# Performance work log

Hardware: AMD Instinct MI355X
Metric: run time of the kernel (lower is better)

## Reference

```python
import jax, jax.numpy as jnp
import numpy as np
import math

H = 12  # heads (init kwarg)
KEEP_RATE = 0.7  # forward arg keep_rate (< 1 -> token pruning path)


def setup_inputs() -> dict:
    key = jax.random.key(0)
    k0, k1, k2 = jax.random.split(key, 3)
    b, n, c = 32, 577, 768  # ViT-B/16 @ 384px: 576 patches + CLS
    x = jax.random.normal(k0, (b, n, c), dtype=jnp.float32)
    # nn.Linear(dim, dim*3) and nn.Linear(dim, dim); kaiming-ish scale
    W_qkv = jax.random.normal(k1, (c, 3 * c), dtype=jnp.float32) / np.sqrt(c).astype(np.float32)
    b_qkv = jnp.zeros((3 * c,), dtype=jnp.float32)
    W_out = jax.random.normal(k2, (c, c), dtype=jnp.float32) / np.sqrt(c).astype(np.float32)
    b_out = jnp.zeros((c,), dtype=jnp.float32)
    return {"x": x, "keep_rate": KEEP_RATE, "W_qkv": W_qkv, "b_qkv": b_qkv,
            "W_out": W_out, "b_out": b_out}


def reference(x, keep_rate, W_qkv, b_qkv, W_out, b_out):
    b, n, c = x.shape
    d = c // H
    scale = (c / H) ** -0.5
    # qkv projection + split into heads: 'b n (h d) -> b h n d'
    qkv = x @ W_qkv + b_qkv                      # [b, n, 3c]
    q, k, v = jnp.split(qkv, 3, axis=-1)
    split_heads = lambda t: t.reshape(b, n, H, d).transpose(0, 2, 1, 3)
    q, k, v = split_heads(q), split_heads(k), split_heads(v)
    dots = jnp.einsum('bhid,bhjd->bhij', q, k) * scale   # [b,h,n,n]
    attention = jax.nn.softmax(dots, axis=-1)
    out = jnp.einsum('bhij,bhjd->bhid', attention, v)    # [b,h,n,d]
    out = out.transpose(0, 2, 1, 3).reshape(b, n, c)     # 'b h n d -> b n (h d)'
    out = out @ W_out + b_out                            # to_out (dropout=0)
    final_tokens = n - 1
    if keep_rate < 1:
        final_tokens = math.ceil(keep_rate * final_tokens)
        # CLS-token attention to patch tokens, averaged over heads
        class_attention = attention[:, :, 0, 1:].mean(axis=1)   # [b, n-1]
        _, ind = jax.lax.top_k(class_attention, final_tokens)    # [b, final_tokens]
        ind = jnp.sort(ind, axis=1)
        index = jnp.broadcast_to(ind[:, :, None], (b, final_tokens, c))
        return (x, index, ind, class_attention, final_tokens)
    return (out, None, None, None, final_tokens)
```

## Files before the change

kernel.cpp:

```cpp
#include <hip/hip_runtime.h>
#include <math.h>

#define BATCH 32
#define NTOK 577
#define NPATCH 576
#define CDIM 768
#define HEADS 12
#define DHEAD 64
#define W3 2304
#define FT 404

#define WS_WTIL  24576
#define WS_DBIAS 319488
#define WS_DOTS  319872

#define O_X      0ULL
#define O_INDEX  14180352ULL
#define O_IND    24109056ULL
#define O_CA     24121984ULL
#define O_FT     24140416ULL

__global__ __launch_bounds__(512) void k_fold(const float* __restrict__ x,
                                              const float* __restrict__ W,
                                              const float* __restrict__ bq,
                                              float* __restrict__ wtil,
                                              float* __restrict__ dbias) {
    __shared__ float x0s[CDIM];
    __shared__ float red[512];
    __shared__ float qs[DHEAD];
    const int b = blockIdx.x, h = blockIdx.y, tid = threadIdx.x;
    if (tid < CDIM / 4)
        ((float4*)x0s)[tid] = ((const float4*)(x + (size_t)b * NTOK * CDIM))[tid];
    __syncthreads();
    {
        const int d = tid & 63, seg = tid >> 6;
        const float* Wq = W + h * DHEAD + d;
        const int c0 = seg * 96;
        float acc = 0.f;
        #pragma unroll 32
        for (int c = c0; c < c0 + 96; c++) acc += x0s[c] * Wq[(size_t)c * W3];
        red[tid] = acc;
    }
    __syncthreads();
    if (tid < DHEAD) {
        float q = red[tid];
        #pragma unroll
        for (int s = 1; s < 8; s++) q += red[tid + s * 64];
        q += bq[h * DHEAD + tid];
        qs[tid] = q;
        float t = q * bq[CDIM + h * DHEAD + tid];
        #pragma unroll
        for (int off = 32; off; off >>= 1) t += __shfl_down(t, off);
        if (tid == 0) dbias[b * HEADS + h] = t;
    }
    __syncthreads();
    for (int c = tid; c < CDIM; c += 512) {
        const float* wr = W + (size_t)c * W3 + CDIM + h * DHEAD;
        float acc = 0.f;
        #pragma unroll
        for (int d = 0; d < DHEAD; d += 4) {
            float4 a = *reinterpret_cast<const float4*>(wr + d);
            acc += a.x * qs[d] + a.y * qs[d + 1] + a.z * qs[d + 2] + a.w * qs[d + 3];
        }
        wtil[((size_t)b * HEADS + h) * CDIM + c] = acc;
    }
}

__global__ __launch_bounds__(256) void k_dots(const float* __restrict__ x,
                                              const float* __restrict__ wtil,
                                              const float* __restrict__ dbias,
                                              float* __restrict__ dots,
                                              float* __restrict__ out0) {
    const int b = blockIdx.x, tid = threadIdx.x;
    const int w = tid >> 6, lane = tid & 63, h0 = w * 3;
    float4 wr[3][3];
    float db[3];
    #pragma unroll
    for (int hh = 0; hh < 3; hh++) {
        #pragma unroll
        for (int i = 0; i < 3; i++)
            wr[hh][i] = *reinterpret_cast<const float4*>(
                wtil + ((size_t)b * HEADS + h0 + hh) * CDIM + i * 256 + lane * 4);
        db[hh] = dbias[b * HEADS + h0 + hh];
    }
    const int jbase = blockIdx.y * 32;
    for (int jj = 0; jj < 32; jj++) {
        const int j = jbase + jj;
        if (j >= NTOK) break;
        const float4* xp = reinterpret_cast<const float4*>(x + ((size_t)b * NTOK + j) * CDIM);
        const float4 a0 = xp[lane], a1 = xp[64 + lane], a2 = xp[128 + lane];
        if (w == 0) {
            float4* op = reinterpret_cast<float4*>(out0 + ((size_t)b * NTOK + j) * CDIM);
            op[lane] = a0; op[64 + lane] = a1; op[128 + lane] = a2;
        }
        float acc[3];
        #pragma unroll
        for (int hh = 0; hh < 3; hh++) acc[hh] = 0.f;
        #pragma unroll
        for (int hh = 0; hh < 3; hh++)
            acc[hh] += a0.x * wr[hh][0].x + a0.y * wr[hh][0].y
                     + a0.z * wr[hh][0].z + a0.w * wr[hh][0].w;
        #pragma unroll
        for (int hh = 0; hh < 3; hh++)
            acc[hh] += a1.x * wr[hh][1].x + a1.y * wr[hh][1].y
                     + a1.z * wr[hh][1].z + a1.w * wr[hh][1].w;
        #pragma unroll
        for (int hh = 0; hh < 3; hh++)
            acc[hh] += a2.x * wr[hh][2].x + a2.y * wr[hh][2].y
                     + a2.z * wr[hh][2].z + a2.w * wr[hh][2].w;
        #pragma unroll
        for (int off = 32; off; off >>= 1)
            #pragma unroll
            for (int hh = 0; hh < 3; hh++) acc[hh] += __shfl_xor(acc[hh], off);
        if (lane == 0) {
            #pragma unroll
            for (int hh = 0; hh < 3; hh++)
                dots[((size_t)b * HEADS + h0 + hh) * NTOK + j] = 0.125f * (acc[hh] + db[hh]);
        }
    }
}

__global__ __launch_bounds__(512) void k_catbc(const float* __restrict__ dots,
                                               float* __restrict__ out,
                                               int write_ft) {
    __shared__ float dl[HEADS * NTOK];
    __shared__ float mh[HEADS], sh[HEADS];
    __shared__ unsigned vals[NPATCH];
    __shared__ unsigned long long segmask[9];
    __shared__ int segoff[9];
    __shared__ int ind_lds[FT];
    const int b = blockIdx.x, y = blockIdx.y, tid = threadIdx.x;
    {
        const float4* s4 = (const float4*)(dots + (size_t)b * HEADS * NTOK);
        float4* d4 = (float4*)dl;
        for (int i = tid; i < HEADS * NTOK / 4; i += 512) d4[i] = s4[i];
    }
    __syncthreads();
    const int w = tid >> 6, lane = tid & 63;
    for (int h = w; h < HEADS; h += 8) {
        const float* row = dl + h * NTOK;
        float m = -3.4e38f;
        for (int j = lane; j < NTOK; j += 64) m = fmaxf(m, row[j]);
        #pragma unroll
        for (int off = 32; off; off >>= 1) m = fmaxf(m, __shfl_xor(m, off));
        float s = 0.f;
        for (int j = lane; j < NTOK; j += 64) s += expf(row[j] - m);
        #pragma unroll
        for (int off = 32; off; off >>= 1) s += __shfl_xor(s, off);
        if (lane == 0) { mh[h] = m; sh[h] = s; }
    }
    __syncthreads();
    for (int t = tid; t < NPATCH; t += 512) {
        float ca = 0.f;
        #pragma unroll
        for (int h = 0; h < HEADS; h++)
            ca += expf(dl[h * NTOK + 1 + t] - mh[h]) / sh[h];
        ca *= (1.f / 12.f);
        if (y == 0) out[O_CA + (size_t)b * NPATCH + t] = ca;
        vals[t] = __float_as_uint(ca);
    }
    __syncthreads();
    {
        const uint4* v4 = (const uint4*)vals;
        for (int s = w; s < 9; s += 8) {
            const int t = s * 64 + lane;
            const unsigned myv = vals[t];
            int rank = 0;
            #pragma unroll 8
            for (int j4 = 0; j4 < NPATCH / 4; j4++) {
                const uint4 vv = v4[j4];
                const int j = j4 * 4;
                rank += (vv.x > myv) || (vv.x == myv && j     < t);
                rank += (vv.y > myv) || (vv.y == myv && j + 1 < t);
                rank += (vv.z > myv) || (vv.z == myv && j + 2 < t);
                rank += (vv.w > myv) || (vv.w == myv && j + 3 < t);
            }
            const unsigned long long mask = __ballot(rank < FT);
            if (lane == 0) segmask[s] = mask;
        }
    }
    __syncthreads();
    if (tid == 0) {
        int acc = 0;
        #pragma unroll
        for (int s = 0; s < 9; s++) { segoff[s] = acc; acc += __popcll(segmask[s]); }
    }
    __syncthreads();
    for (int s = w; s < 9; s += 8) {
        const int t = s * 64 + lane;
        const unsigned long long mask = segmask[s];
        if ((mask >> lane) & 1ull) {
            const int pos = segoff[s] + __popcll(mask & ((1ull << lane) - 1ull));
            ind_lds[pos] = t;
            if (y == 0) out[O_IND + (size_t)b * FT + pos] = (float)t;
        }
    }
    if (y == 0 && b == 0 && tid == 0 && write_ft) out[O_FT] = (float)FT;
    __syncthreads();
    {
        const int nrows = (FT - 1 - y) / 16 + 1;
        const int total = nrows * 192;
        for (int f = tid; f < total; f += 512) {
            const int k = f / 192, cc = f - k * 192;
            const int r = y + k * 16;
            const float v = (float)ind_lds[r];
            float4 o; o.x = v; o.y = v; o.z = v; o.w = v;
            ((float4*)(out + O_INDEX + ((size_t)b * FT + r) * CDIM))[cc] = o;
        }
    }
}

extern "C" void kernel_launch(void* const* d_in, const int* in_sizes, int n_in,
                              void* d_out, int out_size, void* d_ws, size_t ws_size,
                              hipStream_t stream) {
    const float* x  = (const float*)d_in[0];
    const float* W  = (const float*)d_in[2];
    const float* bq = (const float*)d_in[3];
    float* ws = (float*)d_ws;
    float* out = (float*)d_out;

    k_fold<<<dim3(BATCH, HEADS), 512, 0, stream>>>(x, W, bq, ws + WS_WTIL, ws + WS_DBIAS);
    k_dots<<<dim3(BATCH, 19), 256, 0, stream>>>(x, ws + WS_WTIL, ws + WS_DBIAS,
                                                ws + WS_DOTS, out + O_X);
    const int write_ft = (out_size > (int)O_FT) ? 1 : 0;
    k_catbc<<<dim3(BATCH, 16), 512, 0, stream>>>(ws + WS_DOTS, out, write_ft);
}
```

Measured before the change: 246.8 us.

## Double-buffer token loads in k_dots and spread x copy across warps

Restructures k_dots so each block handles 16 tokens in groups of 4. It double-buffers the register loads of x rows so that loads for the next group are issued before computing the current one, and it raises the grid from 19 to 37 blocks per batch. The copy of x to the output is now spread across all four warps instead of warp 0 only, and launch bounds request 3 blocks per SM. The aim is better latency hiding and bandwidth use in this memory-bound kernel, at the cost of higher register pressure from the two 4x3 float4 buffers.

```diff
diff --git a/kernel.cpp b/kernel.cpp
--- a/kernel.cpp
+++ b/kernel.cpp
@@ -66,11 +66,68 @@
     }
 }
 
-__global__ __launch_bounds__(256) void k_dots(const float* __restrict__ x,
-                                              const float* __restrict__ wtil,
-                                              const float* __restrict__ dbias,
-                                              float* __restrict__ dots,
-                                              float* __restrict__ out0) {
+#define LOADG(A, G)                                                               \
+    {                                                                             \
+        _Pragma("unroll")                                                         \
+        for (int u = 0; u < 4; u++) {                                             \
+            const int j = jbase + (G) * 4 + u;                                    \
+            if (j < NTOK) {                                                       \
+                const float4* xp =                                                \
+                    (const float4*)(x + ((size_t)b * NTOK + j) * CDIM);           \
+                A[u][0] = xp[lane]; A[u][1] = xp[64 + lane]; A[u][2] = xp[128 + lane]; \
+            } else {                                                              \
+                A[u][0] = A[u][1] = A[u][2] = make_float4(0.f, 0.f, 0.f, 0.f);    \
+            }                                                                     \
+        }                                                                         \
+    }
+
+#define COMPG(A, G)                                                               \
+    {                                                                             \
+        _Pragma("unroll")                                                         \
+        for (int u = 0; u < 4; u++) {                                             \
+            const int j = jbase + (G) * 4 + u;                                    \
+            if (w == u && j < NTOK) {                                             \
+                float4* op = (float4*)(out0 + ((size_t)b * NTOK + j) * CDIM);     \
+                op[lane] = A[u][0]; op[64 + lane] = A[u][1]; op[128 + lane] = A[u][2]; \
+            }                                                                     \
+        }                                                                         \
+        float acc[4][3];                                                          \
+        _Pragma("unroll")                                                         \
+        for (int u = 0; u < 4; u++) { acc[u][0] = acc[u][1] = acc[u][2] = 0.f; }  \
+        _Pragma("unroll")                                                         \
+        for (int i = 0; i < 3; i++)                                               \
+            _Pragma("unroll")                                                     \
+            for (int u = 0; u < 4; u++)                                           \
+                _Pragma("unroll")                                                 \
+                for (int hh = 0; hh < 3; hh++)                                    \
+                    acc[u][hh] += A[u][i].x * wr[hh][i].x + A[u][i].y * wr[hh][i].y \
+                                + A[u][i].z * wr[hh][i].z + A[u][i].w * wr[hh][i].w; \
+        _Pragma("unroll")                                                         \
+        for (int off = 32; off; off >>= 1)                                        \
+            _Pragma("unroll")                                                     \
+            for (int u = 0; u < 4; u++)                                           \
+                _Pragma("unroll")                                                 \
+                for (int hh = 0; hh < 3; hh++)                                    \
+                    acc[u][hh] += __shfl_xor(acc[u][hh], off);                    \
+        if (lane == 0) {                                                          \
+            _Pragma("unroll")                                                     \
+            for (int u = 0; u < 4; u++) {                                         \
+                const int j = jbase + (G) * 4 + u;                                \
+                if (j < NTOK) {                                                   \
+                    _Pragma("unroll")                                             \
+                    for (int hh = 0; hh < 3; hh++)                                \
+                        dots[((size_t)b * HEADS + h0 + hh) * NTOK + j] =          \
+                            0.125f * (acc[u][hh] + db[hh]);                       \
+                }                                                                 \
+            }                                                                     \
+        }                                                                         \
+    }
+
+__global__ __launch_bounds__(256, 3) void k_dots(const float* __restrict__ x,
+                                                 const float* __restrict__ wtil,
+                                                 const float* __restrict__ dbias,
+                                                 float* __restrict__ dots,
+                                                 float* __restrict__ out0) {
     const int b = blockIdx.x, tid = threadIdx.x;
     const int w = tid >> 6, lane = tid & 63, h0 = w * 3;
     float4 wr[3][3];
@@ -83,41 +140,16 @@
                 wtil + ((size_t)b * HEADS + h0 + hh) * CDIM + i * 256 + lane * 4);
         db[hh] = dbias[b * HEADS + h0 + hh];
     }
-    const int jbase = blockIdx.y * 32;
-    for (int jj = 0; jj < 32; jj++) {
-        const int j = jbase + jj;
-        if (j >= NTOK) break;
-        const float4* xp = reinterpret_cast<const float4*>(x + ((size_t)b * NTOK + j) * CDIM);
-        const float4 a0 = xp[lane], a1 = xp[64 + lane], a2 = xp[128 + lane];
-        if (w == 0) {
-            float4* op = reinterpret_cast<float4*>(out0 + ((size_t)b * NTOK + j) * CDIM);
-            op[lane] = a0; op[64 + lane] = a1; op[128 + lane] = a2;
-        }
-        float acc[3];
-        #pragma unroll
-        for (int hh = 0; hh < 3; hh++) acc[hh] = 0.f;
-        #pragma unroll
-        for (int hh = 0; hh < 3; hh++)
-            acc[hh] += a0.x * wr[hh][0].x + a0.y * wr[hh][0].y
-                     + a0.z * wr[hh][0].z + a0.w * wr[hh][0].w;
-        #pragma unroll
-        for (int hh = 0; hh < 3; hh++)
-            acc[hh] += a1.x * wr[hh][1].x + a1.y * wr[hh][1].y
-                     + a1.z * wr[hh][1].z + a1.w * wr[hh][1].w;
-        #pragma unroll
-        for (int hh = 0; hh < 3; hh++)
-            acc[hh] += a2.x * wr[hh][2].x + a2.y * wr[hh][2].y
-                     + a2.z * wr[hh][2].z + a2.w * wr[hh][2].w;
-        #pragma unroll
-        for (int off = 32; off; off >>= 1)
-            #pragma unroll
-            for (int hh = 0; hh < 3; hh++) acc[hh] += __shfl_xor(acc[hh], off);
-        if (lane == 0) {
-            #pragma unroll
-            for (int hh = 0; hh < 3; hh++)
-                dots[((size_t)b * HEADS + h0 + hh) * NTOK + j] = 0.125f * (acc[hh] + db[hh]);
-        }
-    }
+    const int jbase = blockIdx.y * 16;
+    float4 abuf[4][3], nbuf[4][3];
+    LOADG(abuf, 0);
+    LOADG(nbuf, 1);
+    COMPG(abuf, 0);
+    LOADG(abuf, 2);
+    COMPG(nbuf, 1);
+    LOADG(nbuf, 3);
+    COMPG(abuf, 2);
+    COMPG(nbuf, 3);
 }
 
 __global__ __launch_bounds__(512) void k_catbc(const float* __restrict__ dots,
@@ -220,7 +252,7 @@
     float* out = (float*)d_out;
 
     k_fold<<<dim3(BATCH, HEADS), 512, 0, stream>>>(x, W, bq, ws + WS_WTIL, ws + WS_DBIAS);
-    k_dots<<<dim3(BATCH, 19), 256, 0, stream>>>(x, ws + WS_WTIL, ws + WS_DBIAS,
+    k_dots<<<dim3(BATCH, 37), 256, 0, stream>>>(x, ws + WS_WTIL, ws + WS_DBIAS,
                                                 ws + WS_DOTS, out + O_X);
     const int write_ft = (out_size > (int)O_FT) ? 1 : 0;
     k_catbc<<<dim3(BATCH, 16), 512, 0, stream>>>(ws + WS_DOTS, out, write_ft);
```

After: 234.0 us. -5.2%, faster.
